# Kernel optimization log

Measured on AMD Instinct MI355X. Metric: run time of the kernel, lower is better.

## Reference

```python
import jax, jax.numpy as jnp
import numpy as np

KSIZE = 15
SIGMA = 3.0
PAD = KSIZE // 2


def _gauss_kernel2d():
    g = jnp.arange(KSIZE, dtype=jnp.float32) - KSIZE // 2
    g = jnp.exp(-(g ** 2) / (2.0 * SIGMA * SIGMA))
    g = g / g.sum()
    return g[:, None] * g[None, :]  # [15,15]


def _depthwise_blur(x, k2):
    # x: [B,C,H,W]; 15x15 Gaussian applied per channel (matches per-channel F.conv2d loop)
    C = x.shape[1]
    kernel = jnp.broadcast_to(k2[None, None], (C, 1, KSIZE, KSIZE))
    return jax.lax.conv_general_dilated(
        x, kernel, window_strides=(1, 1), padding=[(PAD, PAD), (PAD, PAD)],
        feature_group_count=C, dimension_numbers=("NCHW", "OIHW", "NCHW"))


def setup_inputs() -> dict:
    key = jax.random.key(0)
    B, C, H, W = 4, 3, 1024, 1024
    x = jax.random.uniform(key, (B, C, H, W), dtype=jnp.float32)
    f32 = lambda v: jnp.asarray(v, dtype=jnp.float32)
    return {
        "x": x,
        "gains": jnp.array([1.1, 1.0, 0.9], dtype=jnp.float32),
        "gamma": f32(0.9),
        "shadow_boost": f32(0.1),
        "highlight_reduce": f32(0.1),
        "brightness": f32(0.05),
        "contrast": f32(1.1),
        "enhance_amount": f32(0.8),
        "softness": f32(0.6),
        "intensity": f32(0.3),
        "rotation": f32(30.0),
        "hardness": f32(2.0),
    }


def reference(x, gains, gamma, shadow_boost, highlight_reduce, brightness,
              contrast, enhance_amount, softness, intensity, rotation, hardness):
    B, C, H, W = x.shape
    k2 = _gauss_kernel2d()

    # WhiteBalanceAdjustment
    x = x * gains.reshape(1, C, 1, 1)
    # ToneCurveAdjustment
    x = jnp.power(x, gamma)
    # ShadowHighlightEnhancement
    hi = jax.nn.sigmoid((x - 0.5) * 10.0)
    x = jnp.clip(x + shadow_boost * (1.0 - hi) - highlight_reduce * hi, 0.0, 1.0)
    # GlobalBrightnessContrastAdjustment
    x = jnp.clip(contrast * (x - 0.5) + 0.5 + brightness, 0.0, 1.0)
    # LocalContrastEnhancement
    local_mean = _depthwise_blur(x, k2)
    x = x + enhance_amount * (x - local_mean)
    # SoftnessFilter
    blurred = _depthwise_blur(x, k2)
    x = softness * blurred + (1.0 - softness) * x
    # GradientNDAdjustment
    ys = jnp.linspace(-1.0, 1.0, H, dtype=jnp.float32)
    xs = jnp.linspace(-1.0, 1.0, W, dtype=jnp.float32)
    grid_y, grid_x = jnp.meshgrid(ys, xs, indexing="ij")
    theta = rotation * (np.pi / 180.0)
    grid_rot = grid_x * jnp.cos(theta) + grid_y * jnp.sin(theta)
    mask = jax.nn.sigmoid(-hardness * grid_rot)[None, None]  # [1,1,H,W]
    x = jnp.clip(x * (1.0 - intensity * mask), 0.0, 1.0)

    return jnp.clip(x, 0.0, 1.0)
```

## Files before the change

### kernel.cpp

```cpp
#include <hip/hip_runtime.h>
#include <math.h>

#define HH 1024
#define WW 1024
#define NPLANES 12
#define PLANE (HH * WW)
#define NTOT (NPLANES * PLANE)

#define TW 64
#define TH 64
#define RH 92
#define RB 78
#define PH 80
#define LDSF (156 * PH)

struct W15 { float w[15]; };

__device__ inline float chain1(float t, float gain, float gamma, float sb,
                               float hr, float br, float ct) {
    t = t * gain;
    t = __builtin_amdgcn_exp2f(gamma * __log2f(t));
    float hi = __fdividef(1.0f, 1.0f + __expf((0.5f - t) * 10.0f));
    t = t + sb * (1.0f - hi) - hr * hi;
    t = fminf(fmaxf(t, 0.0f), 1.0f);
    t = ct * (t - 0.5f) + 0.5f + br;
    return fminf(fmaxf(t, 0.0f), 1.0f);
}

__device__ inline int b1r(int r) { return (r < 64) ? (92 + r) : (r + 14); }
__device__ inline int swq(int pr, int q) { return pr * PH + ((q ^ (pr & 3)) << 2); }
__device__ inline int sws(int pr, int j) {
    return pr * PH + ((((j >> 2) ^ (pr & 3)) << 2) | (j & 3));
}

__device__ inline void dot16(const float* f, const W15& wk, float* o) {
#pragma unroll
    for (int j = 0; j < 16; ++j) {
        float a = 0.0f, b = 0.0f;
#pragma unroll
        for (int k = 0; k < 8; ++k)  a += wk.w[k] * f[j + 1 + k];
#pragma unroll
        for (int k = 8; k < 15; ++k) b += wk.w[k] * f[j + 1 + k];
        o[j] = a + b;
    }
}

__device__ inline float dot15(const float* win, const W15& wk) {
    float a = 0.0f, b = 0.0f;
#pragma unroll
    for (int k = 0; k < 8; ++k)  a += wk.w[k] * win[k];
#pragma unroll
    for (int k = 8; k < 15; ++k) b += wk.w[k] * win[k];
    return a + b;
}

__device__ inline void tile_map(int& p, int& x0, int& y0, bool& edge) {
    int L = (blockIdx.z * gridDim.y + blockIdx.y) * gridDim.x + blockIdx.x;
    int xcd = L & 7;
    int t   = L >> 3;
    int g   = xcd * 384 + t;
    p = g >> 8;
    int w  = g & 255;
    int ty = w >> 4, tx = w & 15;
    x0 = tx * TW; y0 = ty * TH;
    edge = (tx == 0) || (tx == 15) || (ty == 0) || (ty == 15);
}

__global__ __launch_bounds__(256) void k_point(
    const float4* __restrict__ x, float4* __restrict__ o,
    const float* __restrict__ gains,
    const float* __restrict__ pg, const float* __restrict__ psb,
    const float* __restrict__ phr, const float* __restrict__ pbr,
    const float* __restrict__ pct)
{
    int i = blockIdx.x * blockDim.x + threadIdx.x;
    if (i >= NTOT / 4) return;
    int c = ((i * 4) / PLANE) % 3;
    float gain = gains[c];
    float gamma = *pg, sb = *psb, hr = *phr, br = *pbr, ct = *pct;

    float4 v = x[i];
    float* pv = (float*)&v;
#pragma unroll
    for (int j = 0; j < 4; ++j)
        pv[j] = chain1(pv[j], gain, gamma, sb, hr, br, ct);
    o[i] = v;
}

__global__ __launch_bounds__(256, 3) void k_fused(
    const float* __restrict__ x1, float* __restrict__ dst,
    const float* __restrict__ penh,
    const float* __restrict__ psoft, const float* __restrict__ pint,
    const float* __restrict__ prot, const float* __restrict__ phard,
    W15 wk)
{
    __shared__ float lds[LDSF];

    int p, x0, y0; bool edge;
    tile_map(p, x0, y0, edge);
    const int tid = threadIdx.x;
    const int tx  = tid & 63;
    const int ty  = tid >> 6;

    const float* __restrict__ plane = x1 + (size_t)p * PLANE;

#pragma unroll
    for (int it = 0; it < 2; ++it) {
        int u = tid + 256 * it;
        if (u < RH * 5) {
            int r = u / 5, s = u - 5 * r;
            int gy  = y0 - 14 + r;
            int gxa = x0 + 16 * s - 16;
            float f[32];
            if (!edge) {
                const float* rp = plane + (size_t)gy * WW + gxa;
#pragma unroll
                for (int i = 0; i < 8; ++i)
                    *(float4*)&f[4 * i] = *(const float4*)(rp + 4 * i);
            } else {
                bool rowin = (unsigned)gy < HH;
                const float* rp = plane + (size_t)(rowin ? gy : 0) * WW;
#pragma unroll
                for (int e2 = 0; e2 < 32; ++e2) {
                    int gx2 = gxa + e2;
                    f[e2] = (rowin && (unsigned)gx2 < WW) ? rp[gx2] : 0.0f;
                }
            }
            float o[16];
            dot16(f, wk, o);
#pragma unroll
            for (int qq = 0; qq < 4; ++qq)
                *(float4*)&lds[swq(r, 4 * s + qq)] = *(float4*)&o[4 * qq];
        }
    }

    float cc[16];
    {
        const float* pc0 = plane + (size_t)(y0 + ty * 16) * WW + (x0 + tx);
#pragma unroll
        for (int jj = 0; jj < 16; ++jj) cc[jj] = pc0[(size_t)jj * WW];
    }
    __syncthreads();

    if (tid < 240) {
        int j = tid % 80, band = tid / 80;
        int rb0 = band * 28;
        int nj  = (band == 2) ? 22 : 28;
        bool xin = (unsigned)(x0 - 8 + j) < WW;
        float win[15];
#pragma unroll
        for (int k = 0; k < 14; ++k) win[k] = lds[sws(rb0 + k, j)];
#pragma unroll
        for (int jj = 0; jj < 28; ++jj) {
            if (jj < nj) {
                int rl = rb0 + jj;
                win[14] = lds[sws(rl + 14, j)];
                float v = dot15(win, wk);
                if (edge) {
                    int gy = y0 - 7 + rl;
                    if (!((unsigned)gy < HH) || !xin) v = 0.0f;
                }
                lds[sws(b1r(rl), j)] = v;
#pragma unroll
                for (int k = 0; k < 14; ++k) win[k] = win[k + 1];
            }
        }
    }
    __syncthreads();

#pragma unroll
    for (int it = 0; it < 2; ++it) {
        int u = tid + 256 * it;
        if (u < RB * 4) {
            int rb = u >> 2, s = u & 3;
            int pb = b1r(rb);
            float f[32];
#pragma unroll
            for (int i = 0; i < 8; ++i)
                *(float4*)&f[4 * i] = *(const float4*)&lds[swq(pb, 4 * s + i)];
            float o[16];
            dot16(f, wk, o);
#pragma unroll
            for (int qq = 0; qq < 4; ++qq)
                *(float4*)&lds[swq(rb, 4 * s + qq)] = *(float4*)&o[4 * qq];
        }
    }
    __syncthreads();

    const float e     = *penh;
    const float sf    = *psoft;
    const float inten = *pint;
    const float hard  = *phard;
    const float theta = (*prot) * 0.017453292519943295f;
    const float cth = __cosf(theta), sth = __sinf(theta);
    const int   gx    = x0 + tx;
    const float gbase = (-1.0f + 2.0f * (float)gx * (1.0f / (float)(WW - 1))) * cth;
    const float ce    = 1.0f + e;

    float bb[16];
#pragma unroll
    for (int jj = 0; jj < 16; ++jj)
        bb[jj] = lds[sws(b1r(ty * 16 + jj + 7), tx + 8)];

    float win[15];
#pragma unroll
    for (int k = 0; k < 14; ++k) win[k] = lds[sws(ty * 16 + k, tx)];

    float* __restrict__ dstP = dst + (size_t)p * PLANE;
#pragma unroll
    for (int jj = 0; jj < 16; ++jj) {
        win[14] = lds[sws(ty * 16 + jj + 14, tx)];
        float B2  = dot15(win, wk);
        float x2c = ce * cc[jj] - e * bb[jj];
        float bx2 = ce * bb[jj] - e * B2;
        float v   = sf * bx2 + (1.0f - sf) * x2c;
        int   y   = y0 + ty * 16 + jj;
        float gyn = -1.0f + 2.0f * (float)y * (1.0f / (float)(HH - 1));
        float mask = __fdividef(1.0f, 1.0f + __expf(hard * (gbase + gyn * sth)));
        v = v * (1.0f - inten * mask);
        v = fminf(fmaxf(v, 0.0f), 1.0f);
        dstP[(size_t)y * WW + gx] = v;
#pragma unroll
        for (int k = 0; k < 14; ++k) win[k] = win[k + 1];
    }
}

extern "C" void kernel_launch(void* const* d_in, const int* in_sizes, int n_in,
                              void* d_out, int out_size, void* d_ws, size_t ws_size,
                              hipStream_t stream)
{
    const float* x       = (const float*)d_in[0];
    const float* gains   = (const float*)d_in[1];
    const float* p_gamma = (const float*)d_in[2];
    const float* p_sb    = (const float*)d_in[3];
    const float* p_hr    = (const float*)d_in[4];
    const float* p_br    = (const float*)d_in[5];
    const float* p_ct    = (const float*)d_in[6];
    const float* p_enh   = (const float*)d_in[7];
    const float* p_soft  = (const float*)d_in[8];
    const float* p_int   = (const float*)d_in[9];
    const float* p_rot   = (const float*)d_in[10];
    const float* p_hard  = (const float*)d_in[11];

    float* X1 = (float*)d_ws;

    W15 wk;
    {
        double g[15], sum = 0.0;
        for (int i = 0; i < 15; ++i) { double d = (double)(i - 7); g[i] = exp(-d * d / 18.0); sum += g[i]; }
        for (int i = 0; i < 15; ++i) wk.w[i] = (float)(g[i] / sum);
    }

    k_point<<<dim3(NTOT / 4 / 256), dim3(256), 0, stream>>>(
        (const float4*)x, (float4*)X1, gains, p_gamma, p_sb, p_hr, p_br, p_ct);

    dim3 grid(WW / TW, HH / TH, NPLANES);
    k_fused<<<grid, dim3(256), 0, stream>>>(
        X1, (float*)d_out, p_enh, p_soft, p_int, p_rot, p_hard, wk);
}
```

Before: 184.2 us.

## Widen pointwise kernel, vectorize edge loads, rebalance bands, recur gradient mask exponent

The pointwise kernel now handles 8 floats per thread using nontemporal loads and launches half as many threads. Edge tiles in the fused kernel load halos as float4 instead of scalar elements. The vertical blur pass is rebalanced to 26 rows per band, which removes the per-iteration guard. The per-row sigmoid exponent is replaced by a running multiplicative recurrence E*=q, trading a per-row exp for a multiply at some risk of accumulated rounding error.

```diff
diff --git a/kernel.cpp b/kernel.cpp
--- a/kernel.cpp
+++ b/kernel.cpp
@@ -13,6 +13,8 @@
 #define RB 78
 #define PH 80
 #define LDSF (156 * PH)
+
+typedef float vf4 __attribute__((ext_vector_type(4)));
 
 struct W15 { float w[15]; };
 
@@ -67,24 +69,26 @@
 }
 
 __global__ __launch_bounds__(256) void k_point(
-    const float4* __restrict__ x, float4* __restrict__ o,
+    const vf4* __restrict__ x, vf4* __restrict__ o,
     const float* __restrict__ gains,
     const float* __restrict__ pg, const float* __restrict__ psb,
     const float* __restrict__ phr, const float* __restrict__ pbr,
     const float* __restrict__ pct)
 {
     int i = blockIdx.x * blockDim.x + threadIdx.x;
-    if (i >= NTOT / 4) return;
-    int c = ((i * 4) / PLANE) % 3;
+    int c = ((i * 8) / PLANE) % 3;
     float gain = gains[c];
     float gamma = *pg, sb = *psb, hr = *phr, br = *pbr, ct = *pct;
 
-    float4 v = x[i];
-    float* pv = (float*)&v;
-#pragma unroll
-    for (int j = 0; j < 4; ++j)
-        pv[j] = chain1(pv[j], gain, gamma, sb, hr, br, ct);
-    o[i] = v;
+    vf4 v0 = __builtin_nontemporal_load(x + 2 * i);
+    vf4 v1 = __builtin_nontemporal_load(x + 2 * i + 1);
+#pragma unroll
+    for (int j = 0; j < 4; ++j) {
+        v0[j] = chain1(v0[j], gain, gamma, sb, hr, br, ct);
+        v1[j] = chain1(v1[j], gain, gamma, sb, hr, br, ct);
+    }
+    o[2 * i]     = v0;
+    o[2 * i + 1] = v1;
 }
 
 __global__ __launch_bounds__(256, 3) void k_fused(
@@ -121,9 +125,12 @@
                 bool rowin = (unsigned)gy < HH;
                 const float* rp = plane + (size_t)(rowin ? gy : 0) * WW;
 #pragma unroll
-                for (int e2 = 0; e2 < 32; ++e2) {
-                    int gx2 = gxa + e2;
-                    f[e2] = (rowin && (unsigned)gx2 < WW) ? rp[gx2] : 0.0f;
+                for (int i = 0; i < 8; ++i) {
+                    int gq = gxa + 4 * i;
+                    float4 v = make_float4(0.f, 0.f, 0.f, 0.f);
+                    if (rowin && gq >= 0 && gq + 3 < WW)
+                        v = *(const float4*)(rp + gq);
+                    *(float4*)&f[4 * i] = v;
                 }
             }
             float o[16];
@@ -144,26 +151,23 @@
 
     if (tid < 240) {
         int j = tid % 80, band = tid / 80;
-        int rb0 = band * 28;
-        int nj  = (band == 2) ? 22 : 28;
+        int rb0 = band * 26;
         bool xin = (unsigned)(x0 - 8 + j) < WW;
         float win[15];
 #pragma unroll
         for (int k = 0; k < 14; ++k) win[k] = lds[sws(rb0 + k, j)];
 #pragma unroll
-        for (int jj = 0; jj < 28; ++jj) {
-            if (jj < nj) {
-                int rl = rb0 + jj;
-                win[14] = lds[sws(rl + 14, j)];
-                float v = dot15(win, wk);
-                if (edge) {
-                    int gy = y0 - 7 + rl;
-                    if (!((unsigned)gy < HH) || !xin) v = 0.0f;
-                }
-                lds[sws(b1r(rl), j)] = v;
-#pragma unroll
-                for (int k = 0; k < 14; ++k) win[k] = win[k + 1];
+        for (int jj = 0; jj < 26; ++jj) {
+            int rl = rb0 + jj;
+            win[14] = lds[sws(rl + 14, j)];
+            float v = dot15(win, wk);
+            if (edge) {
+                int gy = y0 - 7 + rl;
+                if (!((unsigned)gy < HH) || !xin) v = 0.0f;
             }
+            lds[sws(b1r(rl), j)] = v;
+#pragma unroll
+            for (int k = 0; k < 14; ++k) win[k] = win[k + 1];
         }
     }
     __syncthreads();
@@ -197,6 +201,11 @@
     const float gbase = (-1.0f + 2.0f * (float)gx * (1.0f / (float)(WW - 1))) * cth;
     const float ce    = 1.0f + e;
 
+    const float dstep = 2.0f / (float)(HH - 1);
+    const float gy0n  = -1.0f + (float)(y0 + ty * 16) * dstep;
+    float       E     = __expf(hard * (gbase + gy0n * sth));
+    const float q     = __expf(hard * sth * dstep);
+
     float bb[16];
 #pragma unroll
     for (int jj = 0; jj < 16; ++jj)
@@ -215,8 +224,8 @@
         float bx2 = ce * bb[jj] - e * B2;
         float v   = sf * bx2 + (1.0f - sf) * x2c;
         int   y   = y0 + ty * 16 + jj;
-        float gyn = -1.0f + 2.0f * (float)y * (1.0f / (float)(HH - 1));
-        float mask = __fdividef(1.0f, 1.0f + __expf(hard * (gbase + gyn * sth)));
+        float mask = __fdividef(1.0f, 1.0f + E);
+        E *= q;
         v = v * (1.0f - inten * mask);
         v = fminf(fmaxf(v, 0.0f), 1.0f);
         dstP[(size_t)y * WW + gx] = v;
@@ -251,8 +260,8 @@
         for (int i = 0; i < 15; ++i) wk.w[i] = (float)(g[i] / sum);
     }
 
-    k_point<<<dim3(NTOT / 4 / 256), dim3(256), 0, stream>>>(
-        (const float4*)x, (float4*)X1, gains, p_gamma, p_sb, p_hr, p_br, p_ct);
+    k_point<<<dim3(NTOT / 8 / 256), dim3(256), 0, stream>>>(
+        (const vf4*)x, (vf4*)X1, gains, p_gamma, p_sb, p_hr, p_br, p_ct);
 
     dim3 grid(WW / TW, HH / TH, NPLANES);
     k_fused<<<grid, dim3(256), 0, stream>>>(
```

New measurement: 183.0 us. About the same (-0.6%).
